# Kernel optimization log

Measured on AMD Instinct MI355X. Metric: run time of the kernel, lower is better.

## Reference

```python
import jax, jax.numpy as jnp
import numpy as np


def setup_inputs() -> dict:
    key = jax.random.key(0)
    k1, k2, k3, k4 = jax.random.split(key, 4)
    N, M, D = 4096, 4096, 1024
    H = jax.random.normal(k1, (N, D), dtype=jnp.float32)
    K = jax.random.normal(k2, (M, D), dtype=jnp.float32)
    V = jax.random.normal(k3, (M, D), dtype=jnp.float32)
    attn_mask = jax.random.uniform(k4, (N, M), dtype=jnp.float32)
    return {"H": H, "K": K, "V": V, "attn_mask": attn_mask}


def reference(H, K, V, attn_mask):
    # scores: [N, M] = H @ K^T, scaled by sqrt(d)
    d = H.shape[1]
    scores = jnp.matmul(H, K.T) / jnp.sqrt(jnp.asarray(d, dtype=H.dtype))
    # double softmax with elementwise mask multiply in between
    probs = jax.nn.softmax(jax.nn.softmax(scores, axis=1) * attn_mask, axis=1)
    return jnp.matmul(probs, V)
```

## Files before the change

kernel.cpp:

```cpp
#include <hip/hip_runtime.h>
#include <cstdint>

typedef unsigned short u16;
typedef __bf16 bf16x8 __attribute__((ext_vector_type(8)));
typedef float f32x4 __attribute__((ext_vector_type(4)));
typedef unsigned int u32x4 __attribute__((ext_vector_type(4)));

__device__ __forceinline__ float bf2f(u16 h) {
  union { unsigned int u; float f; } v; v.u = ((unsigned int)h) << 16; return v.f;
}
__device__ __forceinline__ u16 f2bf(float f) {
  union { float f; unsigned int u; } v; v.f = f;
  unsigned int u = v.u;
  return (u16)((u + 0x7FFFu + ((u >> 16) & 1u)) >> 16);
}

__device__ __forceinline__ void ld_lds16(const void* g, void* l) {
  __builtin_amdgcn_global_load_lds(
      (const __attribute__((address_space(1))) unsigned int*)g,
      (__attribute__((address_space(3))) unsigned int*)l, 16, 0, 0);
}

__global__ __launch_bounds__(512, 2) void gemm1_kernel(
    const u16* __restrict__ A, const u16* __restrict__ B,
    u16* __restrict__ S, int ldA, int ldB, int ldC)
{
  __shared__ __align__(16) u16 smem[65536];

  const int tid  = threadIdx.x;
  const int lane = tid & 63;
  const int w    = tid >> 6;
  const int wr   = w >> 2;
  const int wc   = w & 3;
  const int quad = lane >> 4;
  const int cIn  = lane & 15;
  const int lrow   = lane >> 3;
  const int gchunk = (lane & 7) ^ lrow;

  const int flat = blockIdx.x;
  const int xcd  = flat & 7;
  const int i    = flat >> 3;
  const int rowT = (xcd >> 1) * 4 + (i & 3);
  const int colT = (xcd & 1) * 8 + (i >> 2);
  const int rowBlk = rowT * 256;
  const int colBlk = colT * 256;

  f32x4 acc[8][4];
  #pragma unroll
  for (int a = 0; a < 8; ++a)
    #pragma unroll
    for (int b = 0; b < 4; ++b) acc[a][b] = {0.f, 0.f, 0.f, 0.f};

  auto stageA = [&](int buf, int kt2) {
    #pragma unroll
    for (int l = 0; l < 4; ++l) {
      const u16* ga = A + (size_t)(rowBlk + l * 64 + w * 8 + lrow) * ldA
                        + kt2 * 64 + gchunk * 8;
      ld_lds16(ga, &smem[buf * 16384 + l * 4096 + w * 512]);
    }
  };
  auto stageB = [&](int buf, int kt2) {
    #pragma unroll
    for (int l = 0; l < 4; ++l) {
      const u16* gb = B + (size_t)(colBlk + l * 64 + w * 8 + lrow) * ldB
                        + kt2 * 64 + gchunk * 8;
      ld_lds16(gb, &smem[32768 + buf * 16384 + l * 4096 + w * 512]);
    }
  };

  stageA(0, 0);
  stageB(0, 0);
  __syncthreads();

  for (int kt = 0; kt < 16; ++kt) {
    const int cur = kt & 1;
    const int aBase = cur * 16384;
    const int bBase = 32768 + cur * 16384;

    bf16x8 bf[4][2];
    #pragma unroll
    for (int q = 0; q < 4; ++q) {
      if (q == 0) {
        if (kt + 1 < 16) stageA(cur ^ 1, kt + 1);
        #pragma unroll
        for (int ni = 0; ni < 4; ++ni)
          #pragma unroll
          for (int ks = 0; ks < 2; ++ks) {
            int row = wc * 64 + ni * 16 + cIn;
            int ch  = (ks * 4 + quad) ^ (row & 7);
            bf[ni][ks] = *(const bf16x8*)&smem[bBase + row * 64 + ch * 8];
          }
      }
      if (q == 1 && kt + 1 < 16) stageB(cur ^ 1, kt + 1);

      bf16x8 af[2][2];
      #pragma unroll
      for (int m = 0; m < 2; ++m)
        #pragma unroll
        for (int ks = 0; ks < 2; ++ks) {
          int row = wr * 128 + (q * 2 + m) * 16 + cIn;
          int ch  = (ks * 4 + quad) ^ (row & 7);
          af[m][ks] = *(const bf16x8*)&smem[aBase + row * 64 + ch * 8];
        }

      __builtin_amdgcn_s_barrier();
      asm volatile("s_waitcnt lgkmcnt(0)" ::: "memory");
      __builtin_amdgcn_sched_barrier(0);
      __builtin_amdgcn_s_setprio(1);
      #pragma unroll
      for (int m = 0; m < 2; ++m)
        #pragma unroll
        for (int ni = 0; ni < 4; ++ni)
          #pragma unroll
          for (int ks = 0; ks < 2; ++ks)
            acc[q * 2 + m][ni] = __builtin_amdgcn_mfma_f32_16x16x32_bf16(
                af[m][ks], bf[ni][ks], acc[q * 2 + m][ni], 0, 0, 0);
      __builtin_amdgcn_s_setprio(0);
      __builtin_amdgcn_sched_barrier(0);
      if (q < 3) __builtin_amdgcn_s_barrier();
    }
    __syncthreads();
  }

  const float scale = 0.03125f;
  u16* epi = smem;
  #pragma unroll
  for (int R = 0; R < 4; ++R) {
    #pragma unroll
    for (int m01 = 0; m01 < 2; ++m01) {
      int mi = R * 2 + m01;
      #pragma unroll
      for (int ni = 0; ni < 4; ++ni) {
        int col = wc * 64 + ni * 16 + cIn;
        #pragma unroll
        for (int r = 0; r < 4; ++r) {
          int er = wr * 32 + m01 * 16 + quad * 4 + r;
          epi[er * 264 + col] = f2bf(acc[mi][ni][r] * scale);
        }
      }
    }
    __syncthreads();
    #pragma unroll
    for (int it = 0; it < 4; ++it) {
      int idx = it * 512 + tid;
      int er  = idx >> 5;
      int c8  = idx & 31;
      int grow = rowBlk + (er >> 5) * 128 + (R * 2 + ((er >> 4) & 1)) * 16 + (er & 15);
      u32x4 v = *(const u32x4*)&epi[er * 264 + c8 * 8];
      *(u32x4*)&S[(size_t)grow * ldC + colBlk + c8 * 8] = v;
    }
    __syncthreads();
  }
}

__global__ __launch_bounds__(256) void gemm2_kernel(
    const u16* __restrict__ A, const u16* __restrict__ B,
    float* __restrict__ Out, const float* __restrict__ L2,
    int ldA, int ldB, int ldC)
{
  __shared__ __align__(16) u16 As[2 * 64 * 64];
  __shared__ __align__(16) u16 Bs[2 * 128 * 64];

  const int tid  = threadIdx.x;
  const int lane = tid & 63;
  const int w    = tid >> 6;
  const int wrow = w >> 1;
  const int wcol = w & 1;
  const int quad = lane >> 4;
  const int cIn  = lane & 15;

  const int flat = blockIdx.x;
  const int xcd  = flat & 7;
  const int i    = flat >> 3;
  const int rowBlk = (xcd * 8 + (i & 7)) * 64;
  const int colBlk = (i >> 3) * 128;

  const int lrow   = lane >> 3;
  const int gchunk = (lane & 7) ^ lrow;

  f32x4 acc[2][4];
  #pragma unroll
  for (int a = 0; a < 2; ++a)
    #pragma unroll
    for (int b = 0; b < 4; ++b) acc[a][b] = {0.f, 0.f, 0.f, 0.f};

  auto stage = [&](int buf, int kt) {
    int kk = kt * 64;
    #pragma unroll
    for (int t = 0; t < 2; ++t) {
      int rg = w * 2 + t;
      const u16* ga = A + (size_t)(rowBlk + rg * 8 + lrow) * ldA + kk + gchunk * 8;
      ld_lds16(ga, &As[buf * 4096 + rg * 512]);
    }
    #pragma unroll
    for (int t = 0; t < 4; ++t) {
      int rg = w * 4 + t;
      const u16* gb = B + (size_t)(colBlk + rg * 8 + lrow) * ldB + kk + gchunk * 8;
      ld_lds16(gb, &Bs[buf * 8192 + rg * 512]);
    }
  };

  stage(0, 0);
  __syncthreads();

  for (int kt = 0; kt < 64; ++kt) {
    const int cur = kt & 1;
    if (kt + 1 < 64) stage(cur ^ 1, kt + 1);

    #pragma unroll
    for (int ks = 0; ks < 2; ++ks) {
      bf16x8 af[2], bfr[4];
      #pragma unroll
      for (int mi = 0; mi < 2; ++mi) {
        int row = wrow * 32 + mi * 16 + cIn;
        int ch  = (ks * 4 + quad) ^ (row & 7);
        af[mi]  = *(const bf16x8*)&As[cur * 4096 + row * 64 + ch * 8];
      }
      #pragma unroll
      for (int ni = 0; ni < 4; ++ni) {
        int row = wcol * 64 + ni * 16 + cIn;
        int ch  = (ks * 4 + quad) ^ (row & 7);
        bfr[ni] = *(const bf16x8*)&Bs[cur * 8192 + row * 64 + ch * 8];
      }
      #pragma unroll
      for (int mi = 0; mi < 2; ++mi)
        #pragma unroll
        for (int ni = 0; ni < 4; ++ni)
          acc[mi][ni] = __builtin_amdgcn_mfma_f32_16x16x32_bf16(
              af[mi], bfr[ni], acc[mi][ni], 0, 0, 0);
    }
    __syncthreads();
  }

  #pragma unroll
  for (int mi = 0; mi < 2; ++mi) {
    #pragma unroll
    for (int r = 0; r < 4; ++r) {
      int row   = rowBlk + wrow * 32 + mi * 16 + quad * 4 + r;
      float inv = 1.0f / L2[row];
      #pragma unroll
      for (int ni = 0; ni < 4; ++ni) {
        int col = colBlk + wcol * 64 + ni * 16 + cIn;
        __builtin_nontemporal_store(acc[mi][ni][r] * inv,
                                    &Out[(size_t)row * ldC + col]);
      }
    }
  }
}

__global__ __launch_bounds__(256) void prep_kernel(
    const float* __restrict__ H, const float* __restrict__ Kin,
    const float* __restrict__ V, u16* __restrict__ Hb, u16* __restrict__ Kb,
    u16* __restrict__ Vt)
{
  int b = blockIdx.x;
  if (b < 8192) {
    const float* src = (b < 4096) ? H : Kin;
    u16* dst = (b < 4096) ? Hb : Kb;
    int i = (b & 4095) * 256 + threadIdx.x;
    f32x4 v = __builtin_nontemporal_load(&((const f32x4*)src)[i]);
    ushort4 o;
    o.x = f2bf(v.x); o.y = f2bf(v.y); o.z = f2bf(v.z); o.w = f2bf(v.w);
    ((ushort4*)dst)[i] = o;
  } else {
    __shared__ float tile[32][33];
    b -= 8192;
    int c0 = (b & 31) * 32;
    int r0 = (b >> 5) * 32;
    int tx = threadIdx.x & 31, ty = threadIdx.x >> 5;
    #pragma unroll
    for (int s = 0; s < 32; s += 8)
      tile[ty + s][tx] = __builtin_nontemporal_load(
          &V[(size_t)(r0 + ty + s) * 1024 + c0 + tx]);
    __syncthreads();
    #pragma unroll
    for (int s = 0; s < 32; s += 8)
      Vt[(size_t)(c0 + ty + s) * 4096 + r0 + tx] = f2bf(tile[tx][ty + s]);
  }
}

__global__ __launch_bounds__(256) void softmax2_kernel(
    u16* __restrict__ S, const float* __restrict__ mask,
    float* __restrict__ L2, int M)
{
  int row = blockIdx.x;
  u16* srow = S + (size_t)row * M;
  const float* mrow = mask + (size_t)row * M;
  const int base = threadIdx.x * 16;

  u16 sl[16];
  *(uint4*)(sl)     = *(const uint4*)(srow + base);
  *(uint4*)(sl + 8) = *(const uint4*)(srow + base + 8);

  float e[16];
  float s1 = 0.f;
  #pragma unroll
  for (int j = 0; j < 16; ++j) { e[j] = __expf(bf2f(sl[j])); s1 += e[j]; }

  __shared__ float wred[8];
  #pragma unroll
  for (int m = 1; m < 64; m <<= 1) s1 += __shfl_xor(s1, m, 64);
  if ((threadIdx.x & 63) == 0) wred[threadIdx.x >> 6] = s1;
  __syncthreads();
  float inv = 1.0f / (wred[0] + wred[1] + wred[2] + wred[3]);

  float mv[16];
  #pragma unroll
  for (int q = 0; q < 4; ++q) {
    f32x4 m4 = __builtin_nontemporal_load((const f32x4*)(mrow + base + q * 4));
    mv[q * 4 + 0] = m4.x; mv[q * 4 + 1] = m4.y;
    mv[q * 4 + 2] = m4.z; mv[q * 4 + 3] = m4.w;
  }

  float lsum = 0.f;
  #pragma unroll
  for (int j = 0; j < 16; ++j) {
    float p = __expf(e[j] * inv * mv[j]);
    lsum += p;
    sl[j] = f2bf(p);
  }
  *(uint4*)(srow + base)     = *(uint4*)(sl);
  *(uint4*)(srow + base + 8) = *(uint4*)(sl + 8);

  #pragma unroll
  for (int m = 1; m < 64; m <<= 1) lsum += __shfl_xor(lsum, m, 64);
  if ((threadIdx.x & 63) == 0) wred[4 + (threadIdx.x >> 6)] = lsum;
  __syncthreads();
  if (threadIdx.x == 0) L2[row] = wred[4] + wred[5] + wred[6] + wred[7];
}

extern "C" void kernel_launch(void* const* d_in, const int* in_sizes, int n_in,
                              void* d_out, int out_size, void* d_ws, size_t ws_size,
                              hipStream_t stream) {
  const float* H    = (const float*)d_in[0];
  const float* Kin  = (const float*)d_in[1];
  const float* V    = (const float*)d_in[2];
  const float* mask = (const float*)d_in[3];
  float* out = (float*)d_out;

  const int N = 4096, M = 4096, D = 1024;

  char* ws = (char*)d_ws;
  u16*   Hb = (u16*)(ws);
  u16*   Kb = (u16*)(ws + (8ull << 20));
  u16*   Vt = (u16*)(ws + (16ull << 20));
  u16*   S  = (u16*)(ws + (24ull << 20));
  float* L2 = (float*)(ws + (56ull << 20));

  prep_kernel<<<dim3(12288), dim3(256), 0, stream>>>(H, Kin, V, Hb, Kb, Vt);

  gemm1_kernel<<<dim3(256), dim3(512), 0, stream>>>(Hb, Kb, S, D, D, M);

  softmax2_kernel<<<dim3(N), dim3(256), 0, stream>>>(S, mask, L2, M);

  gemm2_kernel<<<dim3(512), dim3(256), 0, stream>>>(S, Vt, out, L2, M, M, D);
}
```

Baseline: 245.9 us.

## Enlarge gemm2 tile to 128x128 with triple-buffered LDS pipeline

```diff
diff --git a/kernel.cpp b/kernel.cpp
--- a/kernel.cpp
+++ b/kernel.cpp
@@ -158,8 +158,7 @@
     float* __restrict__ Out, const float* __restrict__ L2,
     int ldA, int ldB, int ldC)
 {
-  __shared__ __align__(16) u16 As[2 * 64 * 64];
-  __shared__ __align__(16) u16 Bs[2 * 128 * 64];
+  __shared__ __align__(16) u16 smem[49152];
 
   const int tid  = threadIdx.x;
   const int lane = tid & 63;
@@ -168,75 +167,81 @@
   const int wcol = w & 1;
   const int quad = lane >> 4;
   const int cIn  = lane & 15;
+  const int lrow   = lane >> 3;
+  const int gchunk = (lane & 7) ^ lrow;
 
   const int flat = blockIdx.x;
   const int xcd  = flat & 7;
   const int i    = flat >> 3;
-  const int rowBlk = (xcd * 8 + (i & 7)) * 64;
-  const int colBlk = (i >> 3) * 128;
-
-  const int lrow   = lane >> 3;
-  const int gchunk = (lane & 7) ^ lrow;
-
-  f32x4 acc[2][4];
-  #pragma unroll
-  for (int a = 0; a < 2; ++a)
+  const int rowBlk = (xcd * 4 + (i & 3)) * 128;
+  const int colBlk = (i >> 2) * 128;
+
+  f32x4 acc[4][4];
+  #pragma unroll
+  for (int a = 0; a < 4; ++a)
     #pragma unroll
     for (int b = 0; b < 4; ++b) acc[a][b] = {0.f, 0.f, 0.f, 0.f};
 
   auto stage = [&](int buf, int kt) {
     int kk = kt * 64;
     #pragma unroll
-    for (int t = 0; t < 2; ++t) {
-      int rg = w * 2 + t;
-      const u16* ga = A + (size_t)(rowBlk + rg * 8 + lrow) * ldA + kk + gchunk * 8;
-      ld_lds16(ga, &As[buf * 4096 + rg * 512]);
-    }
-    #pragma unroll
     for (int t = 0; t < 4; ++t) {
       int rg = w * 4 + t;
+      const u16* ga = A + (size_t)(rowBlk + rg * 8 + lrow) * ldA + kk + gchunk * 8;
+      ld_lds16(ga, &smem[buf * 8192 + rg * 512]);
       const u16* gb = B + (size_t)(colBlk + rg * 8 + lrow) * ldB + kk + gchunk * 8;
-      ld_lds16(gb, &Bs[buf * 8192 + rg * 512]);
+      ld_lds16(gb, &smem[24576 + buf * 8192 + rg * 512]);
     }
   };
 
   stage(0, 0);
-  __syncthreads();
-
+  stage(1, 1);
+
+  int cur = 0;
   for (int kt = 0; kt < 64; ++kt) {
-    const int cur = kt & 1;
-    if (kt + 1 < 64) stage(cur ^ 1, kt + 1);
-
+    if (kt < 63) asm volatile("s_waitcnt vmcnt(8)" ::: "memory");
+    else         asm volatile("s_waitcnt vmcnt(0)" ::: "memory");
+    __builtin_amdgcn_s_barrier();
+    __builtin_amdgcn_sched_barrier(0);
+
+    if (kt + 2 < 64) {
+      int nb = cur + 2; if (nb >= 3) nb -= 3;
+      stage(nb, kt + 2);
+    }
+
+    const int aBase = cur * 8192;
+    const int bBase = 24576 + cur * 8192;
     #pragma unroll
     for (int ks = 0; ks < 2; ++ks) {
-      bf16x8 af[2], bfr[4];
-      #pragma unroll
-      for (int mi = 0; mi < 2; ++mi) {
-        int row = wrow * 32 + mi * 16 + cIn;
+      bf16x8 af[4], bfr[4];
+      #pragma unroll
+      for (int mi = 0; mi < 4; ++mi) {
+        int row = wrow * 64 + mi * 16 + cIn;
         int ch  = (ks * 4 + quad) ^ (row & 7);
-        af[mi]  = *(const bf16x8*)&As[cur * 4096 + row * 64 + ch * 8];
+        af[mi]  = *(const bf16x8*)&smem[aBase + row * 64 + ch * 8];
       }
       #pragma unroll
       for (int ni = 0; ni < 4; ++ni) {
         int row = wcol * 64 + ni * 16 + cIn;
         int ch  = (ks * 4 + quad) ^ (row & 7);
-        bfr[ni] = *(const bf16x8*)&Bs[cur * 8192 + row * 64 + ch * 8];
-      }
-      #pragma unroll
-      for (int mi = 0; mi < 2; ++mi)
+        bfr[ni] = *(const bf16x8*)&smem[bBase + row * 64 + ch * 8];
+      }
+      #pragma unroll
+      for (int mi = 0; mi < 4; ++mi)
         #pragma unroll
         for (int ni = 0; ni < 4; ++ni)
           acc[mi][ni] = __builtin_amdgcn_mfma_f32_16x16x32_bf16(
               af[mi], bfr[ni], acc[mi][ni], 0, 0, 0);
     }
-    __syncthreads();
-  }
-
-  #pragma unroll
-  for (int mi = 0; mi < 2; ++mi) {
+
+    cur = (cur + 1 == 3) ? 0 : cur + 1;
+  }
+
+  #pragma unroll
+  for (int mi = 0; mi < 4; ++mi) {
     #pragma unroll
     for (int r = 0; r < 4; ++r) {
-      int row   = rowBlk + wrow * 32 + mi * 16 + quad * 4 + r;
+      int row   = rowBlk + wrow * 64 + mi * 16 + quad * 4 + r;
       float inv = 1.0f / L2[row];
       #pragma unroll
       for (int ni = 0; ni < 4; ++ni) {
@@ -353,5 +358,5 @@
 
   softmax2_kernel<<<dim3(N), dim3(256), 0, stream>>>(S, mask, L2, M);
 
-  gemm2_kernel<<<dim3(512), dim3(256), 0, stream>>>(S, Vt, out, L2, M, M, D);
-}
+  gemm2_kernel<<<dim3(256), dim3(256), 0, stream>>>(S, Vt, out, L2, M, M, D);
+}
```

After: 234.6 us. 4.6% less time.
